# Kernel optimization log

Measured on AMD Instinct MI355X. Metric: run time of the kernel, lower is better.

The kernel has to match this reference:

```python
import jax, jax.numpy as jnp
import numpy as np

EMBED_DIM = 2048
NUM_EXPERTS = 16  # num_local_experts + 1 shared global expert
TOP_K = 2


def setup_inputs() -> dict:
    key = jax.random.key(0)
    kx, kw = jax.random.split(key)
    x = jax.random.normal(kx, (8, 4096, EMBED_DIM), dtype=jnp.float32)
    # nn.Linear(embed_dim, total_experts, bias=False) weight: [num_experts, embed_dim]
    bound = 1.0 / np.sqrt(EMBED_DIM)
    gate_w = jax.random.uniform(kw, (NUM_EXPERTS, EMBED_DIM), dtype=jnp.float32,
                                minval=-bound, maxval=bound)
    return {"x": x, "gate_w": gate_w}


def reference(x, gate_w):
    # logits: [B, L, E]
    logits = jnp.einsum("bld,ed->ble", x, gate_w)
    probs = jax.nn.softmax(logits, axis=-1)
    weights, indices = jax.lax.top_k(probs, TOP_K)  # [B, L, K] each
    weights = weights / jnp.sum(weights, axis=-1, keepdims=True)
    return weights, indices
```

## Files before the change

### kernel.cpp

```cpp
#include <hip/hip_runtime.h>
#include <cstdint>

#define EMBED      2048
#define NEXP       16
#define NWAVES     8
#define TOKB       64
#define WINF       128
#define NWIN       (EMBED / WINF)
#define NTOK_TOTAL (8 * 4096)
#define WOFF       (NTOK_TOTAL * 2)
#define PAD        17

__device__ __forceinline__ void g2l16(const float* g, float* l) {
    __builtin_amdgcn_global_load_lds(
        (const __attribute__((address_space(1))) void*)(uintptr_t)g,
        (__attribute__((address_space(3))) void*)(uintptr_t)l,
        16, 0, 0);
}

extern "C" __global__ __launch_bounds__(NWAVES * 64, 4)
void router_kernel(const float* __restrict__ x,
                   const float* __restrict__ gw,
                   float* __restrict__ out)
{
    __shared__ float lds_x[2][TOKB * WINF];
    __shared__ float lds_w[2][NEXP * WINF];

    const int tid  = threadIdx.x;
    const int lane = tid & 63;
    const int W    = __builtin_amdgcn_readfirstlane(tid >> 6);
    const int t0   = blockIdx.x * TOKB;

    float acc[NEXP];
#pragma unroll
    for (int e = 0; e < NEXP; ++e) acc[e] = 0.0f;

    auto stage_x = [&](int win, int buf) {
#pragma unroll
        for (int it = 0; it < 4; ++it) {
            const int G   = it * 512 + tid;
            const int row = G >> 5;
            const int pos = G & 31;
            const int g   = (pos & ~7) | ((pos ^ row) & 7);
            const float* src = x + (size_t)(t0 + row) * EMBED + win * WINF + g * 4;
            g2l16(src, &lds_x[buf][G * 4]);
        }
    };

    auto stage_w = [&](int win, int buf) {
        const int e  = tid >> 5;
        const int wg = tid & 31;
        const float* src = gw + e * EMBED + win * WINF + wg * 4;
        g2l16(src, &lds_w[buf][tid * 4]);
    };

    stage_x(0, 0);
    stage_w(0, 0);
    __syncthreads();

    int cur = 0;
    for (int win = 0; win < NWIN; ++win) {
        if (win + 1 < NWIN) {
            stage_x(win + 1, cur ^ 1);
            stage_w(win + 1, cur ^ 1);
        }

        const float* bx = lds_x[cur];
        const float* bw = lds_w[cur];
#pragma unroll
        for (int j = 0; j < 4; ++j) {
            const int g   = W * 4 + j;
            const int pos = (g & ~7) | ((g ^ lane) & 7);
            const float4 x4 = *(const float4*)&bx[lane * WINF + pos * 4];
#pragma unroll
            for (int e = 0; e < NEXP; ++e) {
                const float4 w4 = *(const float4*)&bw[e * WINF + g * 4];
                acc[e] = fmaf(x4.x, w4.x, acc[e]);
                acc[e] = fmaf(x4.y, w4.y, acc[e]);
                acc[e] = fmaf(x4.z, w4.z, acc[e]);
                acc[e] = fmaf(x4.w, w4.w, acc[e]);
            }
        }
        __syncthreads();
        cur ^= 1;
    }

    float (*part)[TOKB][PAD] = (float (*)[TOKB][PAD])lds_x;
#pragma unroll
    for (int e = 0; e < NEXP; ++e) part[W][lane][e] = acc[e];
    __syncthreads();

    if (tid < TOKB) {
        float tot[NEXP];
#pragma unroll
        for (int e = 0; e < NEXP; ++e) tot[e] = 0.0f;
#pragma unroll
        for (int w = 0; w < NWAVES; ++w) {
#pragma unroll
            for (int e = 0; e < NEXP; ++e) tot[e] += part[w][tid][e];
        }

        float m1 = tot[0]; int i1 = 0;
#pragma unroll
        for (int e = 1; e < NEXP; ++e) {
            if (tot[e] > m1) { m1 = tot[e]; i1 = e; }
        }
        float m2 = -INFINITY; int i2 = 0;
#pragma unroll
        for (int e = 0; e < NEXP; ++e) {
            const bool sel = (e != i1) && (tot[e] > m2);
            if (sel) { m2 = tot[e]; i2 = e; }
        }

        const float ed = __expf(m2 - m1);
        const float w1 = 1.0f / (1.0f + ed);
        const float w2 = 1.0f - w1;

        const int t = t0 + tid;
        out[t * 2 + 0] = w1;
        out[t * 2 + 1] = w2;
        out[WOFF + t * 2 + 0] = (float)i1;
        out[WOFF + t * 2 + 1] = (float)i2;
    }
}

extern "C" void kernel_launch(void* const* d_in, const int* in_sizes, int n_in,
                              void* d_out, int out_size, void* d_ws, size_t ws_size,
                              hipStream_t stream) {
    const float* x  = (const float*)d_in[0];
    const float* gw = (const float*)d_in[1];
    float* out = (float*)d_out;

    const int nblocks = NTOK_TOTAL / TOKB;
    router_kernel<<<dim3(nblocks), dim3(NWAVES * 64), 0, stream>>>(x, gw, out);
}
```

Measured before the change: 59.77 us.

## Deepen LDS pipeline to four buffers with halved window and manual vmcnt waits

Halves the feature window per stage to 64 floats and uses four LDS buffers, keeping three loads in flight ahead of compute. Full __syncthreads are replaced by explicit s_waitcnt vmcnt counts plus s_barrier, so later prefetches stay outstanding while earlier buffers are consumed. Gate weights are now staged with 4-byte global_load_lds instead of 16-byte ones. The aim is to hide HBM latency better in this bandwidth-bound reduction. The costs are more barriers per token of work and more, smaller weight-load instructions. The hand-counted vmcnt values must exactly match the number of loads each thread issues.

Result: slower. 64.66 us (+8.2%).

```diff
diff --git a/kernel.cpp b/kernel.cpp
--- a/kernel.cpp
+++ b/kernel.cpp
@@ -5,8 +5,9 @@
 #define NEXP       16
 #define NWAVES     8
 #define TOKB       64
-#define WINF       128
+#define WINF       64
 #define NWIN       (EMBED / WINF)
+#define NBUF       4
 #define NTOK_TOTAL (8 * 4096)
 #define WOFF       (NTOK_TOTAL * 2)
 #define PAD        17
@@ -17,14 +18,20 @@
         (__attribute__((address_space(3))) void*)(uintptr_t)l,
         16, 0, 0);
 }
+__device__ __forceinline__ void g2l4(const float* g, float* l) {
+    __builtin_amdgcn_global_load_lds(
+        (const __attribute__((address_space(1))) void*)(uintptr_t)g,
+        (__attribute__((address_space(3))) void*)(uintptr_t)l,
+        4, 0, 0);
+}
 
 extern "C" __global__ __launch_bounds__(NWAVES * 64, 4)
 void router_kernel(const float* __restrict__ x,
                    const float* __restrict__ gw,
                    float* __restrict__ out)
 {
-    __shared__ float lds_x[2][TOKB * WINF];
-    __shared__ float lds_w[2][NEXP * WINF];
+    __shared__ float lds_x[NBUF][TOKB * WINF];
+    __shared__ float lds_w[NBUF][NEXP * WINF];
 
     const int tid  = threadIdx.x;
     const int lane = tid & 63;
@@ -37,40 +44,33 @@
 
     auto stage_x = [&](int win, int buf) {
 #pragma unroll
-        for (int it = 0; it < 4; ++it) {
-            const int G   = it * 512 + tid;
-            const int row = G >> 5;
-            const int pos = G & 31;
-            const int g   = (pos & ~7) | ((pos ^ row) & 7);
-            const float* src = x + (size_t)(t0 + row) * EMBED + win * WINF + g * 4;
+        for (int it = 0; it < 2; ++it) {
+            const int G    = it * 512 + tid;
+            const int row  = G >> 4;
+            const int pos  = G & 15;
+            const int gsrc = (pos & 8) | ((pos ^ row) & 7);
+            const float* src = x + (size_t)(t0 + row) * EMBED + win * WINF + gsrc * 4;
             g2l16(src, &lds_x[buf][G * 4]);
         }
     };
 
     auto stage_w = [&](int win, int buf) {
-        const int e  = tid >> 5;
-        const int wg = tid & 31;
-        const float* src = gw + e * EMBED + win * WINF + wg * 4;
-        g2l16(src, &lds_w[buf][tid * 4]);
+#pragma unroll
+        for (int it = 0; it < 2; ++it) {
+            const int q = it * 512 + tid;
+            const int e = q >> 6;
+            const int f = q & 63;
+            g2l4(gw + e * EMBED + win * WINF + f, &lds_w[buf][q]);
+        }
     };
 
-    stage_x(0, 0);
-    stage_w(0, 0);
-    __syncthreads();
-
-    int cur = 0;
-    for (int win = 0; win < NWIN; ++win) {
-        if (win + 1 < NWIN) {
-            stage_x(win + 1, cur ^ 1);
-            stage_w(win + 1, cur ^ 1);
-        }
-
-        const float* bx = lds_x[cur];
-        const float* bw = lds_w[cur];
+    auto compute = [&](int win, int buf) {
+        const float* bx = lds_x[buf];
+        const float* bw = lds_w[buf];
 #pragma unroll
-        for (int j = 0; j < 4; ++j) {
-            const int g   = W * 4 + j;
-            const int pos = (g & ~7) | ((g ^ lane) & 7);
+        for (int j = 0; j < 2; ++j) {
+            const int g   = W * 2 + j;
+            const int pos = (g & 8) | ((g ^ lane) & 7);
             const float4 x4 = *(const float4*)&bx[lane * WINF + pos * 4];
 #pragma unroll
             for (int e = 0; e < NEXP; ++e) {
@@ -81,9 +81,32 @@
                 acc[e] = fmaf(x4.w, w4.w, acc[e]);
             }
         }
-        __syncthreads();
-        cur ^= 1;
+    };
+
+    stage_x(0, 0); stage_w(0, 0);
+    stage_x(1, 1); stage_w(1, 1);
+    stage_x(2, 2); stage_w(2, 2);
+    asm volatile("s_waitcnt vmcnt(8)" ::: "memory");
+    __builtin_amdgcn_s_barrier();
+    asm volatile("" ::: "memory");
+
+    for (int win = 0; win < NWIN - 3; ++win) {
+        stage_x(win + 3, (win + 3) & 3);
+        stage_w(win + 3, (win + 3) & 3);
+        compute(win, win & 3);
+        asm volatile("s_waitcnt vmcnt(8) lgkmcnt(0)" ::: "memory");
+        __builtin_amdgcn_s_barrier();
+        asm volatile("" ::: "memory");
     }
+    compute(NWIN - 3, (NWIN - 3) & 3);
+    asm volatile("s_waitcnt vmcnt(4) lgkmcnt(0)" ::: "memory");
+    __builtin_amdgcn_s_barrier();
+    asm volatile("" ::: "memory");
+    compute(NWIN - 2, (NWIN - 2) & 3);
+    asm volatile("s_waitcnt vmcnt(0) lgkmcnt(0)" ::: "memory");
+    __builtin_amdgcn_s_barrier();
+    asm volatile("" ::: "memory");
+    compute(NWIN - 1, (NWIN - 1) & 3);
 
     float (*part)[TOKB][PAD] = (float (*)[TOKB][PAD])lds_x;
 #pragma unroll
```

## Pre-transpose gate weights and read them via scalar loads instead of LDS

Applied to the files above, without the earlier changes.

Adds a small kernel that transposes the gate weight into workspace as [EMBED][NEXP]. The main kernel drops LDS staging for weights and reads them straight from global memory with wave-uniform indices, which lets them go through scalar loads. This cuts LDS traffic and LDS capacity per block, and the x loads for a window are grouped before the FMAs. In exchange there is an extra kernel launch and more scalar-memory pressure inside the inner loop.

Result: slower. 63.79 us (+6.7%).

```diff
diff --git a/kernel.cpp b/kernel.cpp
--- a/kernel.cpp
+++ b/kernel.cpp
@@ -18,13 +18,19 @@
         16, 0, 0);
 }
 
+extern "C" __global__ __launch_bounds__(256)
+void transpose_w(const float* __restrict__ gw, float* __restrict__ wT) {
+    const int i = blockIdx.x * 256 + threadIdx.x;
+    const int d = i >> 4, e = i & 15;
+    wT[i] = gw[e * EMBED + d];
+}
+
 extern "C" __global__ __launch_bounds__(NWAVES * 64, 4)
 void router_kernel(const float* __restrict__ x,
-                   const float* __restrict__ gw,
+                   const float* __restrict__ wT,
                    float* __restrict__ out)
 {
     __shared__ float lds_x[2][TOKB * WINF];
-    __shared__ float lds_w[2][NEXP * WINF];
 
     const int tid  = threadIdx.x;
     const int lane = tid & 63;
@@ -47,38 +53,38 @@
         }
     };
 
-    auto stage_w = [&](int win, int buf) {
-        const int e  = tid >> 5;
-        const int wg = tid & 31;
-        const float* src = gw + e * EMBED + win * WINF + wg * 4;
-        g2l16(src, &lds_w[buf][tid * 4]);
-    };
-
     stage_x(0, 0);
-    stage_w(0, 0);
     __syncthreads();
 
     int cur = 0;
     for (int win = 0; win < NWIN; ++win) {
-        if (win + 1 < NWIN) {
-            stage_x(win + 1, cur ^ 1);
-            stage_w(win + 1, cur ^ 1);
-        }
+        if (win + 1 < NWIN) stage_x(win + 1, cur ^ 1);
 
         const float* bx = lds_x[cur];
-        const float* bw = lds_w[cur];
+
+        float4 xv[4];
 #pragma unroll
         for (int j = 0; j < 4; ++j) {
             const int g   = W * 4 + j;
             const int pos = (g & ~7) | ((g ^ lane) & 7);
-            const float4 x4 = *(const float4*)&bx[lane * WINF + pos * 4];
+            xv[j] = *(const float4*)&bx[lane * WINF + pos * 4];
+        }
+
 #pragma unroll
-            for (int e = 0; e < NEXP; ++e) {
-                const float4 w4 = *(const float4*)&bw[e * WINF + g * 4];
-                acc[e] = fmaf(x4.x, w4.x, acc[e]);
-                acc[e] = fmaf(x4.y, w4.y, acc[e]);
-                acc[e] = fmaf(x4.z, w4.z, acc[e]);
-                acc[e] = fmaf(x4.w, w4.w, acc[e]);
+        for (int j = 0; j < 4; ++j) {
+            const int g = W * 4 + j;
+#pragma unroll
+            for (int h = 0; h < 2; ++h) {
+                const float* wq = wT + (size_t)(win * WINF + g * 4 + h * 2) * NEXP;
+                float wt[2 * NEXP];
+#pragma unroll
+                for (int i = 0; i < 2 * NEXP; ++i) wt[i] = wq[i];
+                const float c0 = (h == 0) ? xv[j].x : xv[j].z;
+                const float c1 = (h == 0) ? xv[j].y : xv[j].w;
+#pragma unroll
+                for (int e = 0; e < NEXP; ++e) acc[e] = fmaf(c0, wt[e], acc[e]);
+#pragma unroll
+                for (int e = 0; e < NEXP; ++e) acc[e] = fmaf(c1, wt[NEXP + e], acc[e]);
             }
         }
         __syncthreads();
@@ -130,7 +136,10 @@
     const float* x  = (const float*)d_in[0];
     const float* gw = (const float*)d_in[1];
     float* out = (float*)d_out;
+    float* wT  = (float*)d_ws;
+
+    transpose_w<<<dim3((NEXP * EMBED) / 256), dim3(256), 0, stream>>>(gw, wT);
 
     const int nblocks = NTOK_TOTAL / TOKB;
-    router_kernel<<<dim3(nblocks), dim3(NWAVES * 64), 0, stream>>>(x, gw, out);
+    router_kernel<<<dim3(nblocks), dim3(NWAVES * 64), 0, stream>>>(x, wT, out);
 }
```
